# Kernel optimization log

Hardware: AMD Instinct MI355X
Metric: run time of the kernel (lower is better)

The kernel has to match this reference:

```python
import jax, jax.numpy as jnp
import numpy as np

N_NODES = 100000
D = 128
N_EDGES = 640000


def _spmm(edge_index, w, x, n):
    # out[i] = sum over edges (i<-j): w * x[j]
    src, dst = edge_index[0], edge_index[1]
    return jax.ops.segment_sum(w[:, None] * x[dst], src, num_segments=n)


def setup_inputs() -> dict:
    key = jax.random.key(0)
    ks = jax.random.split(key, 8)
    inp = {
        "index_vectors": jax.random.normal(ks[0], (N_NODES, D), dtype=jnp.float32),
        "edge_index1": jax.random.randint(ks[1], (2, N_EDGES), 0, N_NODES, dtype=jnp.int64),
        "w1": jnp.ones((N_EDGES,), dtype=jnp.float32),
        "edge_index2": jax.random.randint(ks[2], (2, N_EDGES), 0, N_NODES, dtype=jnp.int64),
        "w2": jnp.ones((N_EDGES,), dtype=jnp.float32),
        "edge_index3": jax.random.randint(ks[3], (2, N_EDGES), 0, N_NODES, dtype=jnp.int64),
        "w3": jnp.ones((N_EDGES,), dtype=jnp.float32),
        "zeroth": jax.random.uniform(ks[4], (1, 1), dtype=jnp.float32),
        "fst": jax.random.uniform(ks[5], (1, 1), dtype=jnp.float32),
        "snd": jax.random.uniform(ks[6], (1, 1), dtype=jnp.float32),
        "trd": jax.random.uniform(ks[7], (1, 1), dtype=jnp.float32),
    }
    return inp


def reference(index_vectors, edge_index1, w1, edge_index2, w2, edge_index3, w3,
              zeroth, fst, snd, trd):
    n = index_vectors.shape[0]
    # hop-1 context: A @ x
    fst_ctx = _spmm(edge_index1, w1, index_vectors, n)
    # hop-2 context: A^2 @ roll(x, 1, axis=1)   (permute_vecs=True)
    snd_ctx = _spmm(edge_index2, w2, jnp.roll(index_vectors, 1, axis=1), n)
    # hop-3 context: A^3 @ roll(x, 2, axis=1)
    trd_ctx = _spmm(edge_index3, w3, jnp.roll(index_vectors, 2, axis=1), n)

    # relu-normalized scalar order weights (get_orders)
    r0, r1, r2, r3 = (jax.nn.relu(zeroth), jax.nn.relu(fst),
                      jax.nn.relu(snd), jax.nn.relu(trd))
    tot = r0 + r1 + r2 + r3 + 1e-6
    r0, r1, r2, r3 = r0 / tot, r1 / tot, r2 / tot, r3 / tot

    # use_sign=False -> plain weighted combination
    return r0 * index_vectors + r1 * fst_ctx + r2 * snd_ctx + r3 * trd_ctx
```

## Files before the change

kernel.cpp:

```cpp
#include <hip/hip_runtime.h>

#define N_NODES 100000
#define D 128
#define N_EDGES 640000
#define TOT_EDGES (3 * N_EDGES)

#define NB   1024
#define NPB  98
#define BCAP 2304
#define RPT  9
#define OVF_CAP 16384
#define NKEY 512

#define EPBA 2560
#define SETBLKA (N_EDGES / EPBA)
#define BLKA (3 * SETBLKA)
#define EPT2 (EPBA / 256)

#define CAST_BLOCKS ((N_NODES * D / 4 + 255) / 256)

#define WS_OVFCNT 0
#define WS_BCUR   64
#define WS_OVF    65600
#define WS_TMP    327744
#define WS_OFFS   19202112
#define WS_CNTS   19602112
#define WS_XB     20002112
#define WS_TOTAL_FAST 45602112

#ifndef __has_builtin
#define __has_builtin(x) 0
#endif
#if __has_builtin(__builtin_amdgcn_alignbit)
#define ALIGN16(hi, lo) __builtin_amdgcn_alignbit((hi), (lo), 16)
#else
#define ALIGN16(hi, lo) (((hi) << 16) | ((lo) >> 16))
#endif

__device__ __forceinline__ void load_r(const float* z0, const float* z1,
                                       const float* z2, const float* z3,
                                       float& r0, float& r1, float& r2, float& r3) {
    r0 = fmaxf(z0[0], 0.0f);
    r1 = fmaxf(z1[0], 0.0f);
    r2 = fmaxf(z2[0], 0.0f);
    r3 = fmaxf(z3[0], 0.0f);
    float inv = 1.0f / (r0 + r1 + r2 + r3 + 1e-6f);
    r0 *= inv; r1 *= inv; r2 *= inv; r3 *= inv;
}

__device__ __forceinline__ unsigned short bf16rn(float f) {
    unsigned int u = __float_as_uint(f);
    u += 0x7FFFu + ((u >> 16) & 1u);
    return (unsigned short)(u >> 16);
}

__global__ __launch_bounds__(256) void prep_kernel(
        const float* __restrict__ x, ushort* __restrict__ xb,
        const int* __restrict__ ei1, const float* __restrict__ w1,
        const int* __restrict__ ei2, const float* __restrict__ w2,
        const int* __restrict__ ei3, const float* __restrict__ w3,
        const float* __restrict__ z0, const float* __restrict__ z1,
        const float* __restrict__ z2, const float* __restrict__ z3,
        int* __restrict__ bcur, int* __restrict__ ovf_count,
        int4* __restrict__ ovf, int2* __restrict__ tmp) {
    if (blockIdx.x >= BLKA) {
        int i = (blockIdx.x - BLKA) * 256 + threadIdx.x;
        if (i < N_NODES * D / 4) {
            float4 v = ((const float4*)x)[i];
            ushort4 h4;
            h4.x = bf16rn(v.x); h4.y = bf16rn(v.y);
            h4.z = bf16rn(v.z); h4.w = bf16rn(v.w);
            ((ushort4*)xb)[i] = h4;
        }
        return;
    }
    __shared__ int bb[NB];
    __shared__ int h[NB];
    __shared__ int ts[256];
    __shared__ int2 srec[EPBA];
    __shared__ int gx[EPBA];

    int t = threadIdx.x;
    int blk = blockIdx.x;
    for (int i = t; i < NB; i += 256) h[i] = 0;
    __syncthreads();

    float r0, r1, r2, r3;
    load_r(z0, z1, z2, z3, r0, r1, r2, r3);

    int set = blk / SETBLKA;
    int e0  = (blk - set * SETBLKA) * EPBA;
    const int* ei;  const float* w;  float rk;
    if      (set == 0) { ei = ei1; w = w1; rk = r1; }
    else if (set == 1) { ei = ei2; w = w2; rk = r2; }
    else               { ei = ei3; w = w3; rk = r3; }

    int bkt[EPT2], rnk[EPT2], lcl[EPT2], dstv[EPT2];
    float scv[EPT2];
#pragma unroll
    for (int k = 0; k < EPT2; ++k) {
        int idx = e0 + t + k * 256;
        int src = ei[idx];
        dstv[k] = ei[N_EDGES + idx];
        scv[k]  = rk * w[idx];
        int b = src / NPB;
        bkt[k] = b;
        lcl[k] = src - b * NPB;
        rnk[k] = atomicAdd(&h[b], 1);
    }
    __syncthreads();

    int loc[4];
    int tot = 0;
#pragma unroll
    for (int k = 0; k < 4; ++k) { loc[k] = tot; tot += h[4 * t + k]; }
    for (int i = t; i < NB; i += 256) {
        int c = h[i];
        bb[i] = c ? atomicAdd(&bcur[i * 16], c) : 0;
    }
    ts[t] = tot;
    __syncthreads();
    for (int off = 1; off < 256; off <<= 1) {
        int v = (t >= off) ? ts[t - off] : 0;
        __syncthreads();
        ts[t] += v;
        __syncthreads();
    }
    int tb = ts[t] - tot;
    __syncthreads();
#pragma unroll
    for (int k = 0; k < 4; ++k) h[4 * t + k] = tb + loc[k];
    __syncthreads();

#pragma unroll
    for (int k = 0; k < EPT2; ++k) {
        int b = bkt[k];
        int s = h[b] + rnk[k];
        int rx = dstv[k] | (set << 17) | (lcl[k] << 19);
        srec[s] = make_int2(rx, __float_as_int(scv[k]));
        int p = bb[b] + rnk[k];
        if (p < BCAP) {
            gx[s] = b * BCAP + p;
        } else {
            gx[s] = -1;
            int o = atomicAdd(ovf_count, 1);
            if (o < OVF_CAP) ovf[o] = make_int4(b * NPB + lcl[k],
                                               dstv[k] | (set << 17),
                                               __float_as_int(scv[k]), 0);
        }
    }
    __syncthreads();

    for (int s = t; s < EPBA; s += 256) {
        int g = gx[s];
        if (g >= 0) tmp[g] = srec[s];
    }
}

__global__ __launch_bounds__(256) void binB_kernel(
        const int* __restrict__ bcur, int2* __restrict__ tmp,
        int* __restrict__ offs, int* __restrict__ cnts) {
    __shared__ int dH[NKEY];
    __shared__ int ts[256];
    __shared__ int cur[NKEY];
    __shared__ int nb[NPB + 1];
    int b = blockIdx.x;
    int t = threadIdx.x;
    int n = bcur[b * 16];
    if (n > BCAP) n = BCAP;

    int mrx[RPT], mry[RPT];
#pragma unroll
    for (int k = 0; k < RPT; ++k) {
        int i = t + k * 256;
        if (i < n) { int2 r = tmp[(size_t)b * BCAP + i]; mrx[k] = r.x; mry[k] = r.y; }
        else       { mrx[k] = -1; mry[k] = 0; }
    }

    dH[t] = 0; dH[t + 256] = 0;
    __syncthreads();
#pragma unroll
    for (int k = 0; k < RPT; ++k) {
        if (mrx[k] != -1) {
            int key = (((mrx[k] >> 19) & 0x7F) << 2) | ((mrx[k] >> 17) & 3);
            atomicAdd(&dH[key], 1);
        }
    }
    __syncthreads();

    int k0 = dH[2 * t], k1 = dH[2 * t + 1];
    int tot = k0 + k1;
    ts[t] = tot;
    __syncthreads();
    for (int off = 1; off < 256; off <<= 1) {
        int v = (t >= off) ? ts[t - off] : 0;
        __syncthreads();
        ts[t] += v;
        __syncthreads();
    }
    int tb = ts[t] - tot;
    cur[2 * t]     = tb;
    cur[2 * t + 1] = tb + k0;
    __syncthreads();

    if (t <= NPB) nb[t] = (t < NPB) ? cur[t << 2] : n;
    __syncthreads();

#pragma unroll
    for (int k = 0; k < RPT; ++k) {
        if (mrx[k] != -1) {
            int key = (((mrx[k] >> 19) & 0x7F) << 2) | ((mrx[k] >> 17) & 3);
            int pos = atomicAdd(&cur[key], 1);
            tmp[(size_t)b * BCAP + pos] = make_int2(mrx[k], mry[k]);
        }
    }

    if (t < NPB) {
        int node = b * NPB + t;
        if (node < N_NODES) {
            offs[node] = b * BCAP + nb[t];
            cnts[node] = nb[t + 1] - nb[t];
        }
    }
}

#define GB_ACCUM(RX, RY)                                                       \
    {                                                                          \
        const uint4* rowp = (const uint4*)(xb + (size_t)((RX) & 0x1FFFF) * D); \
        uint4 v = rowp[l16];                                                   \
        int sh = ((RX) >> 17) & 3;                                             \
        float sc = __int_as_float(RY);                                         \
        unsigned int pw = (unsigned int)__shfl((int)v.w, prevq);               \
        unsigned int s1x = ALIGN16(v.x, pw);                                   \
        unsigned int s1y = ALIGN16(v.y, v.x);                                  \
        unsigned int s1z = ALIGN16(v.z, v.y);                                  \
        unsigned int s1w = ALIGN16(v.w, v.z);                                  \
        unsigned int u0 = (sh == 0) ? v.x : (sh == 1) ? s1x : pw;              \
        unsigned int u1 = (sh == 0) ? v.y : (sh == 1) ? s1y : v.x;             \
        unsigned int u2 = (sh == 0) ? v.z : (sh == 1) ? s1z : v.y;             \
        unsigned int u3 = (sh == 0) ? v.w : (sh == 1) ? s1w : v.z;             \
        acc0 += sc * __uint_as_float(u0 << 16);                                \
        acc1 += sc * __uint_as_float(u0 & 0xFFFF0000u);                        \
        acc2 += sc * __uint_as_float(u1 << 16);                                \
        acc3 += sc * __uint_as_float(u1 & 0xFFFF0000u);                        \
        acc4 += sc * __uint_as_float(u2 << 16);                                \
        acc5 += sc * __uint_as_float(u2 & 0xFFFF0000u);                        \
        acc6 += sc * __uint_as_float(u3 << 16);                                \
        acc7 += sc * __uint_as_float(u3 & 0xFFFF0000u);                        \
    }

__global__ __launch_bounds__(256) void gatherb_kernel(
        const float* __restrict__ x, const ushort* __restrict__ xb,
        const int* __restrict__ offs, const int* __restrict__ cnts,
        const int2* __restrict__ recs,
        const float* __restrict__ z0, const float* __restrict__ z1,
        const float* __restrict__ z2, const float* __restrict__ z3,
        float* __restrict__ out) {
    int wid  = (blockIdx.x * blockDim.x + threadIdx.x) >> 6;
    int lane = threadIdx.x & 63;
    if (wid >= N_NODES) return;

    float r0, r1, r2, r3;
    load_r(z0, z1, z2, z3, r0, r1, r2, r3);

    int qt    = lane >> 4;
    int l16   = lane & 15;
    int prevq = (qt << 4) | ((l16 + 15) & 15);

    int beg   = offs[wid];
    int count = cnts[wid];
    int cnt64 = (count < 64) ? count : 64;

    int mrx = 0, mry = 0;
    if (lane < cnt64) { int2 rec = recs[beg + lane]; mrx = rec.x; mry = rec.y; }

    float acc0 = 0.f, acc1 = 0.f, acc2 = 0.f, acc3 = 0.f;
    float acc4 = 0.f, acc5 = 0.f, acc6 = 0.f, acc7 = 0.f;

    for (int j = 0; j < cnt64; j += 4) {
        int srcl = j + qt;
        int rx = __shfl(mrx, srcl);
        int ry = __shfl(mry, srcl);
        GB_ACCUM(rx, ry)
    }
    for (int q = 64; q < count; q += 4) {
        int qq = q + qt;
        int rx = 0, ry = 0;
        if (qq < count) { int2 rec = recs[beg + qq]; rx = rec.x; ry = rec.y; }
        GB_ACCUM(rx, ry)
    }

    acc0 += __shfl_xor(acc0, 16); acc0 += __shfl_xor(acc0, 32);
    acc1 += __shfl_xor(acc1, 16); acc1 += __shfl_xor(acc1, 32);
    acc2 += __shfl_xor(acc2, 16); acc2 += __shfl_xor(acc2, 32);
    acc3 += __shfl_xor(acc3, 16); acc3 += __shfl_xor(acc3, 32);
    acc4 += __shfl_xor(acc4, 16); acc4 += __shfl_xor(acc4, 32);
    acc5 += __shfl_xor(acc5, 16); acc5 += __shfl_xor(acc5, 32);
    acc6 += __shfl_xor(acc6, 16); acc6 += __shfl_xor(acc6, 32);
    acc7 += __shfl_xor(acc7, 16); acc7 += __shfl_xor(acc7, 32);

    if (lane < 16) {
        const float4* xr = (const float4*)(x + (size_t)wid * D);
        float4 xlo = xr[2 * l16];
        float4 xhi = xr[2 * l16 + 1];
        float4 olo, ohi;
        olo.x = r0 * xlo.x + acc0;
        olo.y = r0 * xlo.y + acc1;
        olo.z = r0 * xlo.z + acc2;
        olo.w = r0 * xlo.w + acc3;
        ohi.x = r0 * xhi.x + acc4;
        ohi.y = r0 * xhi.y + acc5;
        ohi.z = r0 * xhi.z + acc6;
        ohi.w = r0 * xhi.w + acc7;
        float4* op = (float4*)(out + (size_t)wid * D);
        op[2 * l16]     = olo;
        op[2 * l16 + 1] = ohi;
    }
}

__global__ void ovf_kernel(const float* __restrict__ x,
                           const int* __restrict__ ovf_count,
                           const int4* __restrict__ ovf,
                           float* __restrict__ out) {
    int total_waves = (gridDim.x * blockDim.x) >> 6;
    int gw   = (blockIdx.x * blockDim.x + threadIdx.x) >> 6;
    int lane = threadIdx.x & 63;
    int n = *ovf_count;
    if (n > OVF_CAP) n = OVF_CAP;
    for (int r = gw; r < n; r += total_waves) {
        int4 rec = ovf[r];
        int src = rec.x;
        int dst = rec.y & 0x1FFFF;
        int sh  = (rec.y >> 17) & 3;
        float sc = __int_as_float(rec.z);
        const float* xr = x + (size_t)dst * D;
        float* orow = out + (size_t)src * D;
        int c0 = 2 * lane, c1 = 2 * lane + 1;
        atomicAdd(&orow[c0], sc * xr[(c0 - sh) & 127]);
        atomicAdd(&orow[c1], sc * xr[(c1 - sh) & 127]);
    }
}

#define SCAN_BLOCKS ((N_NODES + 255) / 256)
#define WS_COUNTS   0
#define WS_OFFSETS  400000
#define WS_CURSORS  800008
#define WS_BSUM     1200008
#define WS_BPRE     1201576
#define WS_RECS     1203144
#define WS_NEEDED_MID (WS_RECS + (size_t)TOT_EDGES * 8)

__global__ void hist_kernel(const int* __restrict__ ei1, const int* __restrict__ ei2,
                            const int* __restrict__ ei3, int* __restrict__ counts) {
    int e = blockIdx.x * blockDim.x + threadIdx.x;
    if (e >= TOT_EDGES) return;
    int set = e / N_EDGES;
    int idx = e - set * N_EDGES;
    const int* ei = (set == 0) ? ei1 : (set == 1) ? ei2 : ei3;
    atomicAdd(&counts[ei[idx]], 1);
}

__global__ void scan1_kernel(const int* __restrict__ counts,
                             int* __restrict__ offsets, int* __restrict__ bsum) {
    __shared__ int s[256];
    int t = threadIdx.x;
    int i = blockIdx.x * 256 + t;
    int v = (i < N_NODES) ? counts[i] : 0;
    s[t] = v;
    __syncthreads();
    for (int off = 1; off < 256; off <<= 1) {
        int u = (t >= off) ? s[t - off] : 0;
        __syncthreads();
        s[t] += u;
        __syncthreads();
    }
    if (i < N_NODES) offsets[i] = s[t] - v;
    if (t == 255) bsum[blockIdx.x] = s[255];
}

__global__ void scan2_kernel(const int* __restrict__ bsum, int* __restrict__ bpre) {
    __shared__ int s[512];
    int t = threadIdx.x;
    int v = (t < SCAN_BLOCKS) ? bsum[t] : 0;
    s[t] = v;
    __syncthreads();
    for (int off = 1; off < 512; off <<= 1) {
        int u = (t >= off) ? s[t - off] : 0;
        __syncthreads();
        s[t] += u;
        __syncthreads();
    }
    if (t < SCAN_BLOCKS) bpre[t] = s[t] - v;
}

__global__ void scan3_kernel(int* __restrict__ offsets, const int* __restrict__ bpre,
                             int* __restrict__ cursors) {
    int i = blockIdx.x * 256 + threadIdx.x;
    if (i < N_NODES) {
        int v = offsets[i] + bpre[blockIdx.x];
        offsets[i] = v;
        cursors[i] = v;
    }
    if (i == 0) offsets[N_NODES] = TOT_EDGES;
}

__global__ void fill_kernel(const int* __restrict__ ei1, const float* __restrict__ w1,
                            const int* __restrict__ ei2, const float* __restrict__ w2,
                            const int* __restrict__ ei3, const float* __restrict__ w3,
                            const float* __restrict__ z0, const float* __restrict__ z1,
                            const float* __restrict__ z2, const float* __restrict__ z3,
                            int* __restrict__ cursors, int2* __restrict__ recs) {
    int e = blockIdx.x * blockDim.x + threadIdx.x;
    if (e >= TOT_EDGES) return;
    int set = e / N_EDGES;
    int idx = e - set * N_EDGES;
    const int* ei;  const float* w;
    if      (set == 0) { ei = ei1; w = w1; }
    else if (set == 1) { ei = ei2; w = w2; }
    else               { ei = ei3; w = w3; }
    float r0, r1, r2, r3;
    load_r(z0, z1, z2, z3, r0, r1, r2, r3);
    float rk = (set == 0) ? r1 : (set == 1) ? r2 : r3;
    int src = ei[idx];
    int dst = ei[N_EDGES + idx];
    float scale = rk * w[idx];
    int pos = atomicAdd(&cursors[src], 1);
    recs[pos] = make_int2(dst | (set << 17), __float_as_int(scale));
}

__global__ void gatherd_kernel(const float* __restrict__ x,
                               const int* __restrict__ offsets,
                               const int2* __restrict__ recs,
                               const float* __restrict__ z0, const float* __restrict__ z1,
                               const float* __restrict__ z2, const float* __restrict__ z3,
                               float* __restrict__ out) {
    int wid  = (blockIdx.x * blockDim.x + threadIdx.x) >> 6;
    int lane = threadIdx.x & 63;
    if (wid >= N_NODES) return;
    float r0, r1, r2, r3;
    load_r(z0, z1, z2, z3, r0, r1, r2, r3);
    float2 xv = ((const float2*)(x + (size_t)wid * D))[lane];
    int beg = offsets[wid];
    int end = offsets[wid + 1];
    float2 a0 = {0.f, 0.f}, a1 = {0.f, 0.f}, a2 = {0.f, 0.f};
    for (int j = beg; j < end; ++j) {
        int2 rec = recs[j];
        float2 v = ((const float2*)(x + (size_t)(rec.x & 0x1FFFF) * D))[lane];
        int sh = (rec.x >> 17) & 3;
        float sc = __int_as_float(rec.y);
        if      (sh == 0) { a0.x += sc * v.x; a0.y += sc * v.y; }
        else if (sh == 1) { a1.x += sc * v.x; a1.y += sc * v.y; }
        else               { a2.x += sc * v.x; a2.y += sc * v.y; }
    }
    int prev = (lane + 63) & 63;
    float r1y = __shfl(a1.y, prev);
    float r2x = __shfl(a2.x, prev);
    float r2y = __shfl(a2.y, prev);
    float2 o;
    o.x = r0 * xv.x + a0.x + r1y  + r2x;
    o.y = r0 * xv.y + a0.y + a1.x + r2y;
    ((float2*)(out + (size_t)wid * D))[lane] = o;
}

extern "C" void kernel_launch(void* const* d_in, const int* in_sizes, int n_in,
                              void* d_out, int out_size, void* d_ws, size_t ws_size,
                              hipStream_t stream) {
    const float* x   = (const float*)d_in[0];
    const int*   ei1 = (const int*)  d_in[1];
    const float* w1  = (const float*)d_in[2];
    const int*   ei2 = (const int*)  d_in[3];
    const float* w2  = (const float*)d_in[4];
    const int*   ei3 = (const int*)  d_in[5];
    const float* w3  = (const float*)d_in[6];
    const float* z0  = (const float*)d_in[7];
    const float* z1  = (const float*)d_in[8];
    const float* z2  = (const float*)d_in[9];
    const float* z3  = (const float*)d_in[10];
    float* out = (float*)d_out;
    char* wsc = (char*)d_ws;

    if (ws_size >= WS_TOTAL_FAST) {
        int*    ovf_count = (int*)   (wsc + WS_OVFCNT);
        int*    bcur      = (int*)   (wsc + WS_BCUR);
        int4*   ovf       = (int4*)  (wsc + WS_OVF);
        int2*   tmp       = (int2*)  (wsc + WS_TMP);
        int*    offs      = (int*)   (wsc + WS_OFFS);
        int*    cnts      = (int*)   (wsc + WS_CNTS);
        ushort* xb        = (ushort*)(wsc + WS_XB);

        hipMemsetAsync(wsc, 0, WS_OVF, stream);
        prep_kernel<<<BLKA + CAST_BLOCKS, 256, 0, stream>>>(
            x, xb, ei1, w1, ei2, w2, ei3, w3, z0, z1, z2, z3,
            bcur, ovf_count, ovf, tmp);
        binB_kernel<<<NB, 256, 0, stream>>>(bcur, tmp, offs, cnts);
        gatherb_kernel<<<(N_NODES * 64 + 255) / 256, 256, 0, stream>>>(
            x, xb, offs, cnts, tmp, z0, z1, z2, z3, out);
        ovf_kernel<<<128, 256, 0, stream>>>(x, ovf_count, ovf, out);
    } else {
        int*  counts  = (int*) (wsc + WS_COUNTS);
        int*  offsets = (int*) (wsc + WS_OFFSETS);
        int*  cursors = (int*) (wsc + WS_CURSORS);
        int*  bsum    = (int*) (wsc + WS_BSUM);
        int*  bpre    = (int*) (wsc + WS_BPRE);
        int2* recs    = (int2*)(wsc + WS_RECS);

        hipMemsetAsync(counts, 0, N_NODES * sizeof(int), stream);
        hist_kernel<<<TOT_EDGES / 256, 256, 0, stream>>>(ei1, ei2, ei3, counts);
        scan1_kernel<<<SCAN_BLOCKS, 256, 0, stream>>>(counts, offsets, bsum);
        scan2_kernel<<<1, 512, 0, stream>>>(bsum, bpre);
        scan3_kernel<<<SCAN_BLOCKS, 256, 0, stream>>>(offsets, bpre, cursors);
        fill_kernel<<<TOT_EDGES / 256, 256, 0, stream>>>(ei1, w1, ei2, w2, ei3, w3,
                                                         z0, z1, z2, z3, cursors, recs);
        gatherd_kernel<<<(N_NODES * 64 + 255) / 256, 256, 0, stream>>>(x, offsets, recs,
                                                                       z0, z1, z2, z3, out);
    }
}
```

Baseline: 286.8 us.

## Scatter binned edge records directly to global memory without LDS staging

The prep kernel no longer sorts each block's records in shared memory with a prefix scan before writing them out. Each edge now writes straight to its global bucket slot, which removes the LDS staging buffers, the block scan and several barriers. Edges per block are halved to shorten per-thread work and raise occupancy, the cast path becomes a grid-stride loop over fewer blocks, and the overflow kernel launches fewer blocks. The cost is less coalesced global writes, since records are no longer grouped by bucket before the store.

```diff
diff --git a/kernel.cpp b/kernel.cpp
--- a/kernel.cpp
+++ b/kernel.cpp
@@ -12,12 +12,13 @@
 #define OVF_CAP 16384
 #define NKEY 512
 
-#define EPBA 2560
+#define EPBA 1280
 #define SETBLKA (N_EDGES / EPBA)
 #define BLKA (3 * SETBLKA)
 #define EPT2 (EPBA / 256)
 
-#define CAST_BLOCKS ((N_NODES * D / 4 + 255) / 256)
+#define CASTBLK 1563
+#define GATHER_BLOCKS (N_NODES * 64 / 256)
 
 #define WS_OVFCNT 0
 #define WS_BCUR   64
@@ -64,8 +65,9 @@
         int* __restrict__ bcur, int* __restrict__ ovf_count,
         int4* __restrict__ ovf, int2* __restrict__ tmp) {
     if (blockIdx.x >= BLKA) {
-        int i = (blockIdx.x - BLKA) * 256 + threadIdx.x;
-        if (i < N_NODES * D / 4) {
+        int gid = (blockIdx.x - BLKA) * 256 + threadIdx.x;
+        const int total = CASTBLK * 256;
+        for (int i = gid; i < N_NODES * D / 4; i += total) {
             float4 v = ((const float4*)x)[i];
             ushort4 h4;
             h4.x = bf16rn(v.x); h4.y = bf16rn(v.y);
@@ -74,11 +76,8 @@
         }
         return;
     }
+    __shared__ int h[NB];
     __shared__ int bb[NB];
-    __shared__ int h[NB];
-    __shared__ int ts[256];
-    __shared__ int2 srec[EPBA];
-    __shared__ int gx[EPBA];
 
     int t = threadIdx.x;
     int blk = blockIdx.x;
@@ -95,65 +94,40 @@
     else if (set == 1) { ei = ei2; w = w2; rk = r2; }
     else               { ei = ei3; w = w3; rk = r3; }
 
-    int bkt[EPT2], rnk[EPT2], lcl[EPT2], dstv[EPT2];
+    int bkt[EPT2], rnk[EPT2], rxv[EPT2];
     float scv[EPT2];
 #pragma unroll
     for (int k = 0; k < EPT2; ++k) {
         int idx = e0 + t + k * 256;
         int src = ei[idx];
-        dstv[k] = ei[N_EDGES + idx];
+        int dst = ei[N_EDGES + idx];
         scv[k]  = rk * w[idx];
         int b = src / NPB;
+        int local = src - b * NPB;
         bkt[k] = b;
-        lcl[k] = src - b * NPB;
+        rxv[k] = dst | (set << 17) | (local << 19);
         rnk[k] = atomicAdd(&h[b], 1);
     }
     __syncthreads();
 
-    int loc[4];
-    int tot = 0;
-#pragma unroll
-    for (int k = 0; k < 4; ++k) { loc[k] = tot; tot += h[4 * t + k]; }
     for (int i = t; i < NB; i += 256) {
         int c = h[i];
         bb[i] = c ? atomicAdd(&bcur[i * 16], c) : 0;
     }
-    ts[t] = tot;
-    __syncthreads();
-    for (int off = 1; off < 256; off <<= 1) {
-        int v = (t >= off) ? ts[t - off] : 0;
-        __syncthreads();
-        ts[t] += v;
-        __syncthreads();
-    }
-    int tb = ts[t] - tot;
-    __syncthreads();
-#pragma unroll
-    for (int k = 0; k < 4; ++k) h[4 * t + k] = tb + loc[k];
     __syncthreads();
 
 #pragma unroll
     for (int k = 0; k < EPT2; ++k) {
         int b = bkt[k];
-        int s = h[b] + rnk[k];
-        int rx = dstv[k] | (set << 17) | (lcl[k] << 19);
-        srec[s] = make_int2(rx, __float_as_int(scv[k]));
-        int p = bb[b] + rnk[k];
-        if (p < BCAP) {
-            gx[s] = b * BCAP + p;
+        int pos = bb[b] + rnk[k];
+        if (pos < BCAP) {
+            tmp[(size_t)b * BCAP + pos] = make_int2(rxv[k], __float_as_int(scv[k]));
         } else {
-            gx[s] = -1;
             int o = atomicAdd(ovf_count, 1);
-            if (o < OVF_CAP) ovf[o] = make_int4(b * NPB + lcl[k],
-                                               dstv[k] | (set << 17),
-                                               __float_as_int(scv[k]), 0);
+            int src = b * NPB + ((rxv[k] >> 19) & 0x7F);
+            if (o < OVF_CAP) ovf[o] = make_int4(src, rxv[k] & 0x7FFFF,
+                                                __float_as_int(scv[k]), 0);
         }
-    }
-    __syncthreads();
-
-    for (int s = t; s < EPBA; s += 256) {
-        int g = gx[s];
-        if (g >= 0) tmp[g] = srec[s];
     }
 }
 
@@ -489,13 +463,13 @@
         ushort* xb        = (ushort*)(wsc + WS_XB);
 
         hipMemsetAsync(wsc, 0, WS_OVF, stream);
-        prep_kernel<<<BLKA + CAST_BLOCKS, 256, 0, stream>>>(
+        prep_kernel<<<BLKA + CASTBLK, 256, 0, stream>>>(
             x, xb, ei1, w1, ei2, w2, ei3, w3, z0, z1, z2, z3,
             bcur, ovf_count, ovf, tmp);
         binB_kernel<<<NB, 256, 0, stream>>>(bcur, tmp, offs, cnts);
-        gatherb_kernel<<<(N_NODES * 64 + 255) / 256, 256, 0, stream>>>(
+        gatherb_kernel<<<GATHER_BLOCKS, 256, 0, stream>>>(
             x, xb, offs, cnts, tmp, z0, z1, z2, z3, out);
-        ovf_kernel<<<128, 256, 0, stream>>>(x, ovf_count, ovf, out);
+        ovf_kernel<<<64, 256, 0, stream>>>(x, ovf_count, ovf, out);
     } else {
         int*  counts  = (int*) (wsc + WS_COUNTS);
         int*  offsets = (int*) (wsc + WS_OFFSETS);
```

Result: slower. 299.1 us (+4.3%).
